# Optimization experiments

Hardware: AMD Instinct MI355X
Metric: run time of the kernel (lower is better)

## Reference

```python
import jax, jax.numpy as jnp
from jax import lax
import numpy as np

B, N, C = 8, 32768, 256          # batch, num votes, seed_feat_dim
P, S = 256, 16                   # num_proposal, nsample
RADIUS = 0.3
NH, NS, NC = 1, 18, 18           # heading bins, size clusters, classes
OUT_DIM = 2 + 3 + NH * 2 + NS * 4 + NC  # 97
BN_EPS = 1e-3                    # keras BatchNormalization default epsilon
BN_SCALE = np.float32(1.0 / np.sqrt(1.0 + BN_EPS))  # moving_mean=0, moving_var=1
MEAN_SIZE = ((np.arange(NS * 3, dtype=np.float32).reshape(NS, 3) % 5.0) + 1.0) * 0.2


def _bn(x, g, b):
    # inference-mode BN with moving_mean=0, moving_var=1
    return g * (x * BN_SCALE) + b


def _fps(xyz, npoint):
    # farthest point sampling -> [B, npoint] int32 indices
    b, n = xyz.shape[0], xyz.shape[1]

    def step(carry, _):
        dist, last = carry                                   # [B,N], [B]
        p = jnp.take_along_axis(xyz, last[:, None, None], axis=1)  # [B,1,3]
        d = jnp.sum((xyz - p) ** 2, axis=-1)                 # [B,N]
        dist = jnp.minimum(dist, d)
        nxt = jnp.argmax(dist, axis=1).astype(jnp.int32)
        return (dist, nxt), last

    init = (jnp.full((b, n), 1e10, xyz.dtype), jnp.zeros((b,), jnp.int32))
    _, inds = lax.scan(step, init, None, length=npoint)
    return jnp.transpose(inds)                               # [B, npoint]


def _ball_query(xyz, new_xyz, radius, nsample):
    # first-nsample neighbors within radius, padded with first hit -> [B,P,S]
    n = xyz.shape[1]
    d2 = (jnp.sum(new_xyz ** 2, -1)[:, :, None]
          + jnp.sum(xyz ** 2, -1)[:, None, :]
          - 2.0 * jnp.einsum('bpd,bnd->bpn', new_xyz, xyz))  # [B,P,N]
    key = jnp.where(d2 < radius * radius, jnp.arange(n, dtype=jnp.int32), n)
    sel = -lax.top_k(-key, nsample)[0]                        # ascending smallest
    first = sel[..., :1]                                      # query point itself is always in-radius
    return jnp.where(sel < n, sel, first)


def _forward(xyz, features, mw0, mb0, mg0, me0, mw1, mb1, mg1, me1,
             mw2, mb2, mg2, me2, hw1, hb1, hg1, he1, hw2, hb2, hg2, he2, hw3, hb3):
    fps_inds = _fps(xyz, P)                                           # [B,P]
    new_xyz = jnp.take_along_axis(xyz, fps_inds[..., None], axis=1)   # [B,P,3]
    idx = _ball_query(xyz, new_xyz, RADIUS, S)                        # [B,P,S]

    g_xyz = jax.vmap(lambda pts, i: pts[i])(xyz, idx)                 # [B,P,S,3]
    g_xyz = (g_xyz - new_xyz[:, :, None, :]) / RADIUS                 # normalize_xyz
    g_feat = jax.vmap(lambda f, i: f[i])(features, idx)               # [B,P,S,C]
    h = jnp.concatenate([g_xyz, g_feat], axis=-1)                     # [B,P,S,C+3]

    # shared MLP (conv2d 1x1 + BN + ReLU) then max-pool over samples
    h = jax.nn.relu(_bn(h @ mw0 + mb0, mg0, me0))
    h = jax.nn.relu(_bn(h @ mw1 + mb1, mg1, me1))
    h = jax.nn.relu(_bn(h @ mw2 + mb2, mg2, me2))
    feats = jnp.max(h, axis=2)                                        # [B,P,128]

    # proposal head: conv1x1 + BN + ReLU x2, then conv1x1
    net = jax.nn.relu(_bn(feats @ hw1 + hb1, hg1, he1))
    net = jax.nn.relu(_bn(net @ hw2 + hb2, hg2, he2))
    net = net @ hw3 + hb3                                             # [B,P,97]

    # decode_scores
    obj = net[:, :, 0:2]
    center = new_xyz + net[:, :, 2:5]
    hs = net[:, :, 5:5 + NH]
    hrn = net[:, :, 5 + NH:5 + 2 * NH]
    hr = hrn * (np.pi / NH)
    ss = net[:, :, 5 + 2 * NH:5 + 2 * NH + NS]
    srn = net[:, :, 5 + 2 * NH + NS:5 + 2 * NH + 4 * NS].reshape(net.shape[0], P, NS, 3)
    sr = srn * jnp.asarray(MEAN_SIZE)[None, None]
    sem = net[:, :, 5 + 2 * NH + 4 * NS:]
    return (obj, center, hs, hrn, hr, ss, srn, sr, sem)


def setup_inputs() -> dict:
    key = jax.random.key(0)
    ks = jax.random.split(key, 16)

    def w(k, shape, scale=0.05):
        return jax.random.normal(k, shape, jnp.float32) * scale

    z, o = jnp.zeros, jnp.ones
    return {
        'xyz': jax.random.normal(ks[0], (B, N, 3), jnp.float32),
        'features': jax.random.normal(ks[1], (B, N, C), jnp.float32),
        'mw0': w(ks[2], (C + 3, 128)), 'mb0': z((128,)), 'mg0': o((128,)), 'me0': z((128,)),
        'mw1': w(ks[3], (128, 128)), 'mb1': z((128,)), 'mg1': o((128,)), 'me1': z((128,)),
        'mw2': w(ks[4], (128, 128)), 'mb2': z((128,)), 'mg2': o((128,)), 'me2': z((128,)),
        'hw1': w(ks[5], (128, 128)), 'hb1': z((128,)), 'hg1': o((128,)), 'he1': z((128,)),
        'hw2': w(ks[6], (128, 128)), 'hb2': z((128,)), 'hg2': o((128,)), 'he2': z((128,)),
        'hw3': w(ks[7], (128, OUT_DIM)), 'hb3': z((OUT_DIM,)),
    }


def reference(xyz, features, mw0, mb0, mg0, me0, mw1, mb1, mg1, me1,
              mw2, mb2, mg2, me2, hw1, hb1, hg1, he1, hw2, hb2, hg2, he2, hw3, hb3):
    return _forward(xyz, features, mw0, mb0, mg0, me0, mw1, mb1, mg1, me1,
                    mw2, mb2, mg2, me2, hw1, hb1, hg1, he1, hw2, hb2, hg2, he2, hw3, hb3)
```

## Files before the change

kernel.cpp:

```cpp
#include <hip/hip_runtime.h>
#include <math.h>

#define NBATCH 8
#define NPOINT 32768
#define NFEAT 256
#define NPROP 256
#define NSAMP 16
#define KIN 259
#define HDIM 128
#define ODIM 97

__device__ __forceinline__ float addrn(float a, float b) {
  float r; asm("v_add_f32 %0, %1, %2" : "=v"(r) : "v"(a), "v"(b)); return r;
}
__device__ __forceinline__ float subrn(float a, float b) {
  float r; asm("v_sub_f32 %0, %1, %2" : "=v"(r) : "v"(a), "v"(b)); return r;
}

__global__ __launch_bounds__(256)
void soa_kernel(const float* __restrict__ xyz, float* __restrict__ xs,
                float* __restrict__ ys, float* __restrict__ zs) {
  const int i = blockIdx.x * 256 + threadIdx.x;
  xs[i] = xyz[3*i+0];
  ys[i] = xyz[3*i+1];
  zs[i] = xyz[3*i+2];
}

__global__ __launch_bounds__(1024, 4)
void fps_kernel(const float* __restrict__ xs_, const float* __restrict__ ys_,
                const float* __restrict__ zs_, float* __restrict__ cxyz) {
  __shared__ __align__(16) float dist[NPOINT];
  __shared__ float rv[16];
  __shared__ int ri[16];
  __shared__ int bc;
  const int b = blockIdx.x;
  const int t = threadIdx.x;
  const float* __restrict__ X = xs_ + (size_t)b * NPOINT;
  const float* __restrict__ Y = ys_ + (size_t)b * NPOINT;
  const float* __restrict__ Z = zs_ + (size_t)b * NPOINT;
  float px[32], py[32], pz[32];
#pragma unroll
  for (int q = 0; q < 8; ++q) {
    const int o = q * 4096 + t * 4;
    const float4 vx = *(const float4*)&X[o];
    const float4 vy = *(const float4*)&Y[o];
    const float4 vz = *(const float4*)&Z[o];
    px[q*4+0]=vx.x; px[q*4+1]=vx.y; px[q*4+2]=vx.z; px[q*4+3]=vx.w;
    py[q*4+0]=vy.x; py[q*4+1]=vy.y; py[q*4+2]=vy.z; py[q*4+3]=vy.w;
    pz[q*4+0]=vz.x; pz[q*4+1]=vz.y; pz[q*4+2]=vz.z; pz[q*4+3]=vz.w;
    *(float4*)&dist[o] = make_float4(1e10f, 1e10f, 1e10f, 1e10f);
  }
  __syncthreads();
  int last = 0;
  for (int step = 0; step < NPROP; ++step) {
    const float qx = X[last];
    const float qy = Y[last];
    const float qz = Z[last];
    if (t == 0) {
      cxyz[(b*NPROP+step)*3+0] = qx;
      cxyz[(b*NPROP+step)*3+1] = qy;
      cxyz[(b*NPROP+step)*3+2] = qz;
    }
    float bv = -1.0f; int bi = 0;
#pragma unroll
    for (int q = 0; q < 8; ++q) {
      const int o = q * 4096 + t * 4;
      float4 dv = *(float4*)&dist[o];
      float* dp = (float*)&dv;
#pragma unroll
      for (int u = 0; u < 4; ++u) {
        const int j = q*4+u;
        const float dx = px[j]-qx, dy = py[j]-qy, dz = pz[j]-qz;
        const float d = addrn(addrn(dx*dx, dy*dy), dz*dz);
        const float nd = fminf(dp[u], d);
        dp[u] = nd;
        if (nd > bv) { bv = nd; bi = o + u; }
      }
      *(float4*)&dist[o] = dv;
    }
#pragma unroll
    for (int m = 1; m < 64; m <<= 1) {
      const float ov = __shfl_xor(bv, m);
      const int   oi = __shfl_xor(bi, m);
      if (ov > bv || (ov == bv && oi < bi)) { bv = ov; bi = oi; }
    }
    if ((t & 63) == 0) { rv[t >> 6] = bv; ri[t >> 6] = bi; }
    __syncthreads();
    if (t < 64) {
      float fv = (t < 16) ? rv[t] : -2.0f;
      int   fi = (t < 16) ? ri[t] : 0x7fffffff;
#pragma unroll
      for (int m = 1; m < 16; m <<= 1) {
        const float ov = __shfl_xor(fv, m);
        const int   oi = __shfl_xor(fi, m);
        if (ov > fv || (ov == fv && oi < fi)) { fv = ov; fi = oi; }
      }
      if (t == 0) bc = fi;
    }
    __syncthreads();
    last = bc;
  }
}

__global__ __launch_bounds__(512)
void ballq_kernel(const float* __restrict__ xs_, const float* __restrict__ ys_,
                  const float* __restrict__ zs_, const float* __restrict__ cxyz,
                  int* __restrict__ idx) {
  const int gw = (blockIdx.x * 512 + threadIdx.x) >> 6;
  const int lane = threadIdx.x & 63;
  const int b = gw >> 8;
  const float* __restrict__ X = xs_ + (size_t)b * NPOINT;
  const float* __restrict__ Y = ys_ + (size_t)b * NPOINT;
  const float* __restrict__ Z = zs_ + (size_t)b * NPOINT;
  const float cx = cxyz[gw*3+0], cy = cxyz[gw*3+1], cz = cxyz[gw*3+2];
  const float a = addrn(addrn(cx*cx, cy*cy), cz*cz);
  const float R2 = (float)(0.3 * 0.3);
  int* __restrict__ out = idx + gw * NSAMP;
  int cnt = 0, first = -1;
  for (int base = 0; base < NPOINT; base += 64) {
    const int i = base + lane;
    const float x = X[i], y = Y[i], z = Z[i];
    const float bb2 = addrn(addrn(x*x, y*y), z*z);
    const float cc  = addrn(addrn(cx*x, cy*y), cz*z);
    const float d2  = subrn(addrn(a, bb2), 2.0f*cc);
    const bool isin = d2 < R2;
    const unsigned long long m = __ballot(isin);
    if (m) {
      if (first < 0) first = base + (int)__builtin_ctzll(m);
      if (isin) {
        const int pos = cnt + (int)__builtin_popcountll(m & ((1ull << lane) - 1ull));
        if (pos < NSAMP) out[pos] = i;
      }
      cnt += (int)__builtin_popcountll(m);
      if (cnt >= NSAMP) break;
    }
  }
  if (lane < NSAMP && lane >= cnt) out[lane] = first;
}

__global__ __launch_bounds__(256)
void mlp0_kernel(const float* __restrict__ xyz, const float* __restrict__ feat,
                 const float* __restrict__ cxyz, const int* __restrict__ idx,
                 const float* __restrict__ W, const float* __restrict__ bias_,
                 const float* __restrict__ gam_, const float* __restrict__ bet_,
                 float* __restrict__ h0) {
  __shared__ __align__(16) float w[KIN*132];
  __shared__ __align__(16) float xs[16*264];
  __shared__ int ids[16];
  const int t = threadIdx.x;
  for (int i = t; i < KIN*HDIM; i += 256) {
    const int k = i >> 7, c = i & 127;
    w[k*132 + c] = W[i];
  }
  const int r  = t >> 4;
  const int c8 = (t & 15) * 8;
  float bs[8], gm[8], bt[8];
#pragma unroll
  for (int j = 0; j < 8; ++j) { bs[j] = bias_[c8+j]; gm[j] = gam_[c8+j]; bt[j] = bet_[c8+j]; }
  const float bns = (float)(1.0 / sqrt(1.001));
  for (int gi = 0; gi < 8; ++gi) {
    const int g = blockIdx.x * 8 + gi;
    const int b = g >> 8;
    __syncthreads();
    if (t < 16) ids[t] = idx[g*16 + t];
    __syncthreads();
#pragma unroll
    for (int s = 0; s < 16; ++s)
      xs[s*264 + 3 + t] = feat[((size_t)b*NPOINT + ids[s])*NFEAT + t];
    if (t < 48) {
      const int s = t / 3, d = t - 3*(t/3);
      const float v = xyz[((size_t)b*NPOINT + ids[s])*3 + d];
      xs[s*264 + d] = (v - cxyz[g*3 + d]) / 0.3f;
    }
    __syncthreads();
    float acc[8];
#pragma unroll
    for (int j = 0; j < 8; ++j) acc[j] = bs[j];
    for (int k = 0; k < KIN; ++k) {
      const float xv = xs[r*264 + k];
      const float4 wa = *(const float4*)&w[k*132 + c8];
      const float4 wb = *(const float4*)&w[k*132 + c8 + 4];
      acc[0] += xv*wa.x; acc[1] += xv*wa.y; acc[2] += xv*wa.z; acc[3] += xv*wa.w;
      acc[4] += xv*wb.x; acc[5] += xv*wb.y; acc[6] += xv*wb.z; acc[7] += xv*wb.w;
    }
    float ov[8];
#pragma unroll
    for (int j = 0; j < 8; ++j) ov[j] = fmaxf(gm[j]*(acc[j]*bns)+bt[j], 0.0f);
    float* dst = &h0[((size_t)g*16 + r)*HDIM + c8];
    *(float4*)&dst[0] = make_float4(ov[0],ov[1],ov[2],ov[3]);
    *(float4*)&dst[4] = make_float4(ov[4],ov[5],ov[6],ov[7]);
  }
}

__global__ __launch_bounds__(256)
void mlp12_kernel(const float* __restrict__ h0,
                  const float* __restrict__ W1, const float* __restrict__ b1,
                  const float* __restrict__ g1, const float* __restrict__ e1,
                  const float* __restrict__ W2, const float* __restrict__ b2,
                  const float* __restrict__ g2, const float* __restrict__ e2,
                  float* __restrict__ feats) {
  __shared__ __align__(16) float w1[HDIM*132];
  __shared__ __align__(16) float w2[HDIM*132];
  __shared__ __align__(16) float xs[16*132];
  __shared__ __align__(16) float ys[16*132];
  const int t = threadIdx.x;
  for (int i = t; i < HDIM*HDIM; i += 256) {
    const int k = i >> 7, c = i & 127;
    w1[k*132+c] = W1[i];
    w2[k*132+c] = W2[i];
  }
  const int r  = t >> 4;
  const int c8 = (t & 15) * 8;
  float bs1[8], gm1[8], bt1[8], bs2[8], gm2[8], bt2[8];
#pragma unroll
  for (int j = 0; j < 8; ++j) {
    bs1[j]=b1[c8+j]; gm1[j]=g1[c8+j]; bt1[j]=e1[c8+j];
    bs2[j]=b2[c8+j]; gm2[j]=g2[c8+j]; bt2[j]=e2[c8+j];
  }
  const float bns = (float)(1.0 / sqrt(1.001));
  for (int gi = 0; gi < 8; ++gi) {
    const int g = blockIdx.x * 8 + gi;
    __syncthreads();
    for (int i = t; i < 16*HDIM; i += 256) {
      const int s = i >> 7, k = i & 127;
      xs[s*132+k] = h0[((size_t)g*16 + s)*HDIM + k];
    }
    __syncthreads();
    float acc[8];
#pragma unroll
    for (int j = 0; j < 8; ++j) acc[j] = bs1[j];
#pragma unroll 4
    for (int k = 0; k < HDIM; ++k) {
      const float xv = xs[r*132 + k];
      const float4 wa = *(const float4*)&w1[k*132 + c8];
      const float4 wb = *(const float4*)&w1[k*132 + c8 + 4];
      acc[0]+=xv*wa.x; acc[1]+=xv*wa.y; acc[2]+=xv*wa.z; acc[3]+=xv*wa.w;
      acc[4]+=xv*wb.x; acc[5]+=xv*wb.y; acc[6]+=xv*wb.z; acc[7]+=xv*wb.w;
    }
    {
      float ov[8];
#pragma unroll
      for (int j = 0; j < 8; ++j) ov[j] = fmaxf(gm1[j]*(acc[j]*bns)+bt1[j], 0.0f);
      *(float4*)&ys[r*132 + c8]     = make_float4(ov[0],ov[1],ov[2],ov[3]);
      *(float4*)&ys[r*132 + c8 + 4] = make_float4(ov[4],ov[5],ov[6],ov[7]);
    }
    __syncthreads();
#pragma unroll
    for (int j = 0; j < 8; ++j) acc[j] = bs2[j];
#pragma unroll 4
    for (int k = 0; k < HDIM; ++k) {
      const float xv = ys[r*132 + k];
      const float4 wa = *(const float4*)&w2[k*132 + c8];
      const float4 wb = *(const float4*)&w2[k*132 + c8 + 4];
      acc[0]+=xv*wa.x; acc[1]+=xv*wa.y; acc[2]+=xv*wa.z; acc[3]+=xv*wa.w;
      acc[4]+=xv*wb.x; acc[5]+=xv*wb.y; acc[6]+=xv*wb.z; acc[7]+=xv*wb.w;
    }
    {
      float ov[8];
#pragma unroll
      for (int j = 0; j < 8; ++j) ov[j] = fmaxf(gm2[j]*(acc[j]*bns)+bt2[j], 0.0f);
      *(float4*)&xs[r*132 + c8]     = make_float4(ov[0],ov[1],ov[2],ov[3]);
      *(float4*)&xs[r*132 + c8 + 4] = make_float4(ov[4],ov[5],ov[6],ov[7]);
    }
    __syncthreads();
#pragma unroll
    for (int hh = 8; hh >= 1; hh >>= 1) {
      if (r < hh) {
#pragma unroll
        for (int j = 0; j < 8; ++j)
          xs[r*132 + c8 + j] = fmaxf(xs[r*132 + c8 + j], xs[(r+hh)*132 + c8 + j]);
      }
      __syncthreads();
    }
    if (r == 0) {
      *(float4*)&feats[(size_t)g*HDIM + c8]     = *(float4*)&xs[c8];
      *(float4*)&feats[(size_t)g*HDIM + c8 + 4] = *(float4*)&xs[c8+4];
    }
  }
}

__global__ __launch_bounds__(256)
void head_kernel(const float* __restrict__ in_, const float* __restrict__ W,
                 const float* __restrict__ b_, const float* __restrict__ g_,
                 const float* __restrict__ e_, float* __restrict__ out_) {
  __shared__ __align__(16) float w[HDIM*132];
  __shared__ __align__(16) float xs[16*132];
  const int t = threadIdx.x;
  for (int i = t; i < HDIM*HDIM; i += 256) {
    const int k = i >> 7, c = i & 127;
    w[k*132+c] = W[i];
  }
  const int row0 = blockIdx.x * 16;
  for (int i = t; i < 16*HDIM; i += 256) {
    const int s = i >> 7, k = i & 127;
    xs[s*132+k] = in_[((size_t)row0 + s)*HDIM + k];
  }
  const int r  = t >> 4;
  const int c8 = (t & 15) * 8;
  float bs[8], gm[8], bt[8];
#pragma unroll
  for (int j = 0; j < 8; ++j) { bs[j]=b_[c8+j]; gm[j]=g_[c8+j]; bt[j]=e_[c8+j]; }
  const float bns = (float)(1.0 / sqrt(1.001));
  __syncthreads();
  float acc[8];
#pragma unroll
  for (int j = 0; j < 8; ++j) acc[j] = bs[j];
#pragma unroll 4
  for (int k = 0; k < HDIM; ++k) {
    const float xv = xs[r*132 + k];
    const float4 wa = *(const float4*)&w[k*132 + c8];
    const float4 wb = *(const float4*)&w[k*132 + c8 + 4];
    acc[0]+=xv*wa.x; acc[1]+=xv*wa.y; acc[2]+=xv*wa.z; acc[3]+=xv*wa.w;
    acc[4]+=xv*wb.x; acc[5]+=xv*wb.y; acc[6]+=xv*wb.z; acc[7]+=xv*wb.w;
  }
  float ov[8];
#pragma unroll
  for (int j = 0; j < 8; ++j) ov[j] = fmaxf(gm[j]*(acc[j]*bns)+bt[j], 0.0f);
  float* dst = &out_[((size_t)row0 + r)*HDIM + c8];
  *(float4*)&dst[0] = make_float4(ov[0],ov[1],ov[2],ov[3]);
  *(float4*)&dst[4] = make_float4(ov[4],ov[5],ov[6],ov[7]);
}

__global__ __launch_bounds__(128)
void head3_kernel(const float* __restrict__ net2, const float* __restrict__ W3,
                  const float* __restrict__ b3, const float* __restrict__ cxyz,
                  float* __restrict__ out) {
  __shared__ float x[HDIM];
  const int g = blockIdx.x;
  const int t = threadIdx.x;
  x[t] = net2[(size_t)g*HDIM + t];
  __syncthreads();
  if (t >= ODIM) return;
  float acc = b3[t];
#pragma unroll 4
  for (int k = 0; k < HDIM; ++k) acc += x[k] * W3[k*ODIM + t];
  const int OBJ=0, CEN=4096, HSo=10240, HRN=12288, HRo=14336,
            SSo=16384, SRN=53248, SRo=163840, SEM=274432;
  if (t < 2)       out[OBJ + g*2 + t] = acc;
  else if (t < 5)  out[CEN + g*3 + (t-2)] = acc + cxyz[g*3 + (t-2)];
  else if (t == 5) out[HSo + g] = acc;
  else if (t == 6) { out[HRN + g] = acc; out[HRo + g] = acc * (float)M_PI; }
  else if (t < 25) out[SSo + g*18 + (t-7)] = acc;
  else if (t < 79) {
    const int m2 = t - 25;
    out[SRN + g*54 + m2] = acc;
    out[SRo + g*54 + m2] = acc * ((float)(m2 % 5 + 1) * 0.2f);
  }
  else             out[SEM + g*18 + (t-79)] = acc;
}

extern "C" void kernel_launch(void* const* d_in, const int* in_sizes, int n_in,
                              void* d_out, int out_size, void* d_ws, size_t ws_size,
                              hipStream_t stream) {
  (void)in_sizes; (void)n_in; (void)out_size; (void)ws_size;
  const float* xyz  = (const float*)d_in[0];
  const float* feat = (const float*)d_in[1];
  const float* mw0 = (const float*)d_in[2];
  const float* mb0 = (const float*)d_in[3];
  const float* mg0 = (const float*)d_in[4];
  const float* me0 = (const float*)d_in[5];
  const float* mw1 = (const float*)d_in[6];
  const float* mb1 = (const float*)d_in[7];
  const float* mg1 = (const float*)d_in[8];
  const float* me1 = (const float*)d_in[9];
  const float* mw2 = (const float*)d_in[10];
  const float* mb2 = (const float*)d_in[11];
  const float* mg2 = (const float*)d_in[12];
  const float* me2 = (const float*)d_in[13];
  const float* hw1 = (const float*)d_in[14];
  const float* hb1 = (const float*)d_in[15];
  const float* hg1 = (const float*)d_in[16];
  const float* he1 = (const float*)d_in[17];
  const float* hw2 = (const float*)d_in[18];
  const float* hb2 = (const float*)d_in[19];
  const float* hg2 = (const float*)d_in[20];
  const float* he2 = (const float*)d_in[21];
  const float* hw3 = (const float*)d_in[22];
  const float* hb3 = (const float*)d_in[23];
  float* out = (float*)d_out;
  char* ws = (char*)d_ws;
  float* cxyz = (float*)(ws + 8192);
  int*   idx  = (int*)(ws + 32768);
  float* h0   = (float*)(ws + 163840);
  float* xs   = (float*)(ws + 163840);
  float* ys   = (float*)(ws + 163840 + 1048576);
  float* zs   = (float*)(ws + 163840 + 2097152);
  float* fts  = (float*)(ws + 16941056);
  float* net1 = (float*)(ws + 17989632);
  float* net2 = (float*)(ws + 19038208);

  soa_kernel<<<1024, 256, 0, stream>>>(xyz, xs, ys, zs);
  fps_kernel<<<NBATCH, 1024, 0, stream>>>(xs, ys, zs, cxyz);
  ballq_kernel<<<256, 512, 0, stream>>>(xs, ys, zs, cxyz, idx);
  mlp0_kernel<<<256, 256, 0, stream>>>(xyz, feat, cxyz, idx, mw0, mb0, mg0, me0, h0);
  mlp12_kernel<<<256, 256, 0, stream>>>(h0, mw1, mb1, mg1, me1, mw2, mb2, mg2, me2, fts);
  head_kernel<<<128, 256, 0, stream>>>(fts, hw1, hb1, hg1, he1, net1);
  head_kernel<<<128, 256, 0, stream>>>(net1, hw2, hb2, hg2, he2, net2);
  head3_kernel<<<2048, 128, 0, stream>>>(net2, hw3, hb3, cxyz, out);
}
```

Measured before the change: 1.309 ms.

## Halve FPS block size, double points per thread, track argmax per lane component

The farthest-point-sampling kernel now runs 512 threads per batch instead of 1024, so each thread keeps 64 points in registers as float4 vectors. Argmax tracking keeps four independent best-value/group pairs, one per float4 component, using selects instead of branches, which shortens the serial dependency chain. The cross-wave reduction handles 8 waves instead of 16, which means less barrier and reduction work per iteration. The cost is higher register pressure and more serial work per thread in a latency-bound sequential loop.

```diff
diff --git a/kernel.cpp b/kernel.cpp
--- a/kernel.cpp
+++ b/kernel.cpp
@@ -26,30 +26,47 @@
   zs[i] = xyz[3*i+2];
 }
 
-__global__ __launch_bounds__(1024, 4)
+#define FPS_DECL(g) float4 px##g, py##g, pz##g;
+#define FPS_LOAD(g) \
+  px##g = *(const float4*)&X[(g)*2048 + t4]; \
+  py##g = *(const float4*)&Y[(g)*2048 + t4]; \
+  pz##g = *(const float4*)&Z[(g)*2048 + t4]; \
+  dist4[(g)*512 + t] = make_float4(1e10f, 1e10f, 1e10f, 1e10f);
+#define FPS_UPD(c, g) { \
+  const float dx = px##g.c - qx, dy = py##g.c - qy, dz = pz##g.c - qz; \
+  const float d = addrn(addrn(dx*dx, dy*dy), dz*dz); \
+  const float nd = fminf(dv.c, d); \
+  dv.c = nd; \
+  const bool gt = nd > bv_##c;                \
+  bv_##c = gt ? nd : bv_##c; \
+  bg_##c = gt ? (g) : bg_##c; }
+#define FPS_STEP(g) { \
+  float4 dv = dist4[(g)*512 + t]; \
+  FPS_UPD(x, g) FPS_UPD(y, g) FPS_UPD(z, g) FPS_UPD(w, g) \
+  dist4[(g)*512 + t] = dv; }
+
+__global__ __launch_bounds__(512)
+__attribute__((amdgpu_waves_per_eu(2, 2)))
 void fps_kernel(const float* __restrict__ xs_, const float* __restrict__ ys_,
                 const float* __restrict__ zs_, float* __restrict__ cxyz) {
-  __shared__ __align__(16) float dist[NPOINT];
-  __shared__ float rv[16];
-  __shared__ int ri[16];
+  __shared__ __align__(16) float4 dist4[NPOINT/4];
+  __shared__ float rv[8];
+  __shared__ int ri[8];
   __shared__ int bc;
   const int b = blockIdx.x;
   const int t = threadIdx.x;
+  const int t4 = t * 4;
   const float* __restrict__ X = xs_ + (size_t)b * NPOINT;
   const float* __restrict__ Y = ys_ + (size_t)b * NPOINT;
   const float* __restrict__ Z = zs_ + (size_t)b * NPOINT;
-  float px[32], py[32], pz[32];
-#pragma unroll
-  for (int q = 0; q < 8; ++q) {
-    const int o = q * 4096 + t * 4;
-    const float4 vx = *(const float4*)&X[o];
-    const float4 vy = *(const float4*)&Y[o];
-    const float4 vz = *(const float4*)&Z[o];
-    px[q*4+0]=vx.x; px[q*4+1]=vx.y; px[q*4+2]=vx.z; px[q*4+3]=vx.w;
-    py[q*4+0]=vy.x; py[q*4+1]=vy.y; py[q*4+2]=vy.z; py[q*4+3]=vy.w;
-    pz[q*4+0]=vz.x; pz[q*4+1]=vz.y; pz[q*4+2]=vz.z; pz[q*4+3]=vz.w;
-    *(float4*)&dist[o] = make_float4(1e10f, 1e10f, 1e10f, 1e10f);
-  }
+  FPS_DECL(0)  FPS_DECL(1)  FPS_DECL(2)  FPS_DECL(3)
+  FPS_DECL(4)  FPS_DECL(5)  FPS_DECL(6)  FPS_DECL(7)
+  FPS_DECL(8)  FPS_DECL(9)  FPS_DECL(10) FPS_DECL(11)
+  FPS_DECL(12) FPS_DECL(13) FPS_DECL(14) FPS_DECL(15)
+  FPS_LOAD(0)  FPS_LOAD(1)  FPS_LOAD(2)  FPS_LOAD(3)
+  FPS_LOAD(4)  FPS_LOAD(5)  FPS_LOAD(6)  FPS_LOAD(7)
+  FPS_LOAD(8)  FPS_LOAD(9)  FPS_LOAD(10) FPS_LOAD(11)
+  FPS_LOAD(12) FPS_LOAD(13) FPS_LOAD(14) FPS_LOAD(15)
   __syncthreads();
   int last = 0;
   for (int step = 0; step < NPROP; ++step) {
@@ -61,23 +78,19 @@
       cxyz[(b*NPROP+step)*3+1] = qy;
       cxyz[(b*NPROP+step)*3+2] = qz;
     }
-    float bv = -1.0f; int bi = 0;
-#pragma unroll
-    for (int q = 0; q < 8; ++q) {
-      const int o = q * 4096 + t * 4;
-      float4 dv = *(float4*)&dist[o];
-      float* dp = (float*)&dv;
-#pragma unroll
-      for (int u = 0; u < 4; ++u) {
-        const int j = q*4+u;
-        const float dx = px[j]-qx, dy = py[j]-qy, dz = pz[j]-qz;
-        const float d = addrn(addrn(dx*dx, dy*dy), dz*dz);
-        const float nd = fminf(dp[u], d);
-        dp[u] = nd;
-        if (nd > bv) { bv = nd; bi = o + u; }
-      }
-      *(float4*)&dist[o] = dv;
-    }
+    float bv_x = -1.0f, bv_y = -1.0f, bv_z = -1.0f, bv_w = -1.0f;
+    int   bg_x = 0,     bg_y = 0,     bg_z = 0,     bg_w = 0;
+    FPS_STEP(0)  FPS_STEP(1)  FPS_STEP(2)  FPS_STEP(3)
+    FPS_STEP(4)  FPS_STEP(5)  FPS_STEP(6)  FPS_STEP(7)
+    FPS_STEP(8)  FPS_STEP(9)  FPS_STEP(10) FPS_STEP(11)
+    FPS_STEP(12) FPS_STEP(13) FPS_STEP(14) FPS_STEP(15)
+    float bv = bv_x; int bi = bg_x*2048 + t4 + 0;
+    { const int oi = bg_y*2048 + t4 + 1;
+      if (bv_y > bv || (bv_y == bv && oi < bi)) { bv = bv_y; bi = oi; } }
+    { const int oi = bg_z*2048 + t4 + 2;
+      if (bv_z > bv || (bv_z == bv && oi < bi)) { bv = bv_z; bi = oi; } }
+    { const int oi = bg_w*2048 + t4 + 3;
+      if (bv_w > bv || (bv_w == bv && oi < bi)) { bv = bv_w; bi = oi; } }
 #pragma unroll
     for (int m = 1; m < 64; m <<= 1) {
       const float ov = __shfl_xor(bv, m);
@@ -87,10 +100,10 @@
     if ((t & 63) == 0) { rv[t >> 6] = bv; ri[t >> 6] = bi; }
     __syncthreads();
     if (t < 64) {
-      float fv = (t < 16) ? rv[t] : -2.0f;
-      int   fi = (t < 16) ? ri[t] : 0x7fffffff;
-#pragma unroll
-      for (int m = 1; m < 16; m <<= 1) {
+      float fv = (t < 8) ? rv[t] : -2.0f;
+      int   fi = (t < 8) ? ri[t] : 0x7fffffff;
+#pragma unroll
+      for (int m = 1; m < 8; m <<= 1) {
         const float ov = __shfl_xor(fv, m);
         const int   oi = __shfl_xor(fi, m);
         if (ov > fv || (ov == fv && oi < fi)) { fv = ov; fi = oi; }
@@ -390,7 +403,7 @@
   float* net2 = (float*)(ws + 19038208);
 
   soa_kernel<<<1024, 256, 0, stream>>>(xyz, xs, ys, zs);
-  fps_kernel<<<NBATCH, 1024, 0, stream>>>(xs, ys, zs, cxyz);
+  fps_kernel<<<NBATCH, 512, 0, stream>>>(xs, ys, zs, cxyz);
   ballq_kernel<<<256, 512, 0, stream>>>(xs, ys, zs, cxyz, idx);
   mlp0_kernel<<<256, 256, 0, stream>>>(xyz, feat, cxyz, idx, mw0, mb0, mg0, me0, h0);
   mlp12_kernel<<<256, 256, 0, stream>>>(h0, mw1, mb1, mg1, me1, mw2, mb2, mg2, me2, fts);
```

Result: slower. 1.438 ms (+9.9%).
